# Kernel optimization log

Measured on AMD Instinct MI355X. Metric: run time of the kernel, lower is better.

Reference implementation:

```python
import jax, jax.numpy as jnp
import numpy as np

B, L, C, N, TN = 1, 256, 128, 4, 4
CH = N * C  # 512, flattened hidden for routing projections
EPS = 1.1920929e-07  # torch.finfo(float32).eps (RMSNorm default eps)
LN_EPS = 1e-5
N_SINKHORN = 20  # training-mode iteration count


def sinkhorn_knopp(raw, n_iters):
    # raw: [..., n, n] real-valued logits -> doubly-stochastic matrix
    M = jnp.exp(raw)
    for _ in range(n_iters):
        M = M / jnp.sum(M, axis=-1, keepdims=True)  # row normalize
        M = M / jnp.sum(M, axis=-2, keepdims=True)  # col normalize
    return M


def setup_inputs() -> dict:
    key = jax.random.key(0)
    ks = jax.random.split(key, 8)
    s = 0.02
    eye = jnp.eye(N, dtype=jnp.float32)
    b_res = 2.0 * eye + (-2.0) * (1.0 - eye)
    return {
        "p": jax.random.normal(ks[0], (B, L, L, C), jnp.float32),
        "p_mask": jnp.ones((B, L, L), jnp.float32),
        "W_pre": jax.random.normal(ks[1], (N, CH), jnp.float32) * s,
        "W_post": jax.random.normal(ks[2], (N, CH), jnp.float32) * s,
        "W_res": jax.random.normal(ks[3], (N * N, CH), jnp.float32) * s,
        "b_pre": jnp.zeros((1, N), jnp.float32),
        "b_post": jnp.zeros((1, N), jnp.float32),
        "b_res": b_res,
        "alpha_pre": jnp.asarray(0.01, jnp.float32),
        "alpha_post": jnp.asarray(0.01, jnp.float32),
        "alpha_res": jnp.asarray(0.01, jnp.float32),
        "ln_g": jnp.ones((C,), jnp.float32),
        "ln_b": jnp.zeros((C,), jnp.float32),
        "W1": jax.random.normal(ks[4], (TN * C, C), jnp.float32) * s,
        "b1": jnp.zeros((TN * C,), jnp.float32),
        "W2": jax.random.normal(ks[5], (C, TN * C), jnp.float32) * s,
        "b2": jnp.zeros((C,), jnp.float32),
    }


def reference(p, p_mask, W_pre, W_post, W_res, b_pre, b_post, b_res,
              alpha_pre, alpha_post, alpha_res, ln_g, ln_b, W1, b1, W2, b2):
    # expand_input: [B,L,L,C] -> [B,L,L,n,C]
    x = jnp.broadcast_to(p[..., None, :], (B, L, L, N, C))
    # --- compute_mappings ---
    xf = x.reshape(B, L, L, CH)
    xn = xf * jax.lax.rsqrt(jnp.mean(xf * xf, axis=-1, keepdims=True) + EPS)
    H_pre_dyn = jnp.tanh(xn @ W_pre.T)                      # [B,L,L,n]
    H_post_dyn = jnp.tanh(xn @ W_post.T)                    # [B,L,L,n]
    H_res_dyn = jnp.tanh(xn @ W_res.T).reshape(B, L, L, N, N)
    H_pre = jax.nn.sigmoid(alpha_pre * H_pre_dyn + b_pre)   # [B,L,L,n]
    H_post = 2.0 * jax.nn.sigmoid(alpha_post * H_post_dyn + b_post)
    H_res = sinkhorn_knopp(alpha_res * H_res_dyn + b_res, N_SINKHORN)  # [B,L,L,n,n]
    # contract: H_pre [B,L,L,1,n] @ x [B,L,L,n,C] -> [B,L,L,C]
    p_c = jnp.einsum('blkn,blknc->blkc', H_pre, x)
    # --- PairTransition (LN -> Linear -> ReLU -> Linear, masked) ---
    mu = jnp.mean(p_c, axis=-1, keepdims=True)
    var = jnp.mean(jnp.square(p_c - mu), axis=-1, keepdims=True)
    m = (p_c - mu) * jax.lax.rsqrt(var + LN_EPS) * ln_g + ln_b
    h = jax.nn.relu(m @ W1.T + b1)                          # [B,L,L,TN*C]
    p_t = (h @ W2.T + b2) * p_mask[..., None]
    p_updated = p_c + p_t
    # expand back: H_post^T [B,L,L,n,1] * p_updated [B,L,L,1,C]
    p_expanded = H_post[..., :, None] * p_updated[..., None, :]
    # residual mixing: [B,L,L,n,n] @ [B,L,L,n,C]
    p_residual = jnp.einsum('blkmn,blknc->blkmc', H_res, x)
    return p_residual + p_expanded  # [B,L,L,n,C]
```

## Files before the change

### kernel.cpp

```cpp
#include <hip/hip_runtime.h>
#include <stdint.h>

#define LLTOT 65536
#define CDIM  128
#define TPIX  32

typedef float f32x4  __attribute__((ext_vector_type(4)));
typedef float f32x16 __attribute__((ext_vector_type(16)));
typedef short s16x8  __attribute__((ext_vector_type(8)));

#define MFMA16(a, b, c) __builtin_amdgcn_mfma_f32_16x16x32_bf16((a), (b), (c), 0, 0, 0)
#define MFMA32(a, b, c) __builtin_amdgcn_mfma_f32_32x32x16_bf16((a), (b), (c), 0, 0, 0)

#define RPAD 132

__device__ __align__(16) unsigned short g_wefff[2 * 4 * 64 * 8];
__device__ __align__(16) unsigned short g_w1gf[32 * 4 * 64 * 8];
__device__ __align__(16) unsigned short g_w2f [4 * 32 * 64 * 8];
__device__ __align__(16) float  g_hA[512];
__device__ __align__(16) float  g_w1gs[512];

__device__ __forceinline__ unsigned short f2bf(float f) {
    union { float f; uint32_t u; } v; v.f = f;
    uint32_t u = v.u;
    return (unsigned short)((u + 0x7FFFu + ((u >> 16) & 1u)) >> 16);
}
__device__ __forceinline__ uint32_t pack2(float a, float b) {
    uint32_t r;
    asm("v_cvt_pk_bf16_f32 %0, %1, %2" : "=v"(r) : "v"(a), "v"(b));
    return r;
}
__device__ __forceinline__ float bf2f(uint32_t lo16) { return __uint_as_float(lo16 << 16); }

__device__ __forceinline__ float fast_tanh(float x) {
    float cx = fminf(fmaxf(x, -10.f), 10.f);
    float e = __expf(2.f * cx);
    return (e - 1.f) * __builtin_amdgcn_rcpf(e + 1.f);
}
__device__ __forceinline__ float fast_sig(float z) {
    return __builtin_amdgcn_rcpf(1.f + __expf(-z));
}

__global__ void prep_kernel(const float* __restrict__ Wpre, const float* __restrict__ Wpost,
                            const float* __restrict__ Wres, const float* __restrict__ W1,
                            const float* __restrict__ W2, const float* __restrict__ ln_g,
                            const float* __restrict__ ln_b, const float* __restrict__ b1) {
    int b = blockIdx.x, t = threadIdx.x;
    if (b == 264) {
        int j = t;
        float sg = 0.f, sb = 0.f;
        const float* row = W1 + j * 128;
        #pragma unroll 4
        for (int c = 0; c < 128; c += 4) {
            float4 wv = *(const float4*)(row + c);
            float4 gv = *(const float4*)(ln_g + c);
            float4 bv = *(const float4*)(ln_b + c);
            sg += wv.x*gv.x + wv.y*gv.y + wv.z*gv.z + wv.w*gv.w;
            sb += wv.x*bv.x + wv.y*bv.y + wv.z*bv.z + wv.w*bv.w;
        }
        g_hA[j]   = b1[j] + sb;
        g_w1gs[j] = sg;
        return;
    }
    int idx = b * 512 + t;
    if (idx < 4096) {
        int e = idx & 7, lane = (idx >> 3) & 63, kk = (idx >> 9) & 3, tile = idx >> 11;
        int o = tile * 16 + (lane & 15);
        int c = kk * 32 + (lane >> 4) * 8 + e;
        float v = 0.f;
        if (o < 4)        v = Wpre[o*512+c] + Wpre[o*512+128+c] + Wpre[o*512+256+c] + Wpre[o*512+384+c];
        else if (o < 8)   { int j = o - 4;  v = Wpost[j*512+c] + Wpost[j*512+128+c] + Wpost[j*512+256+c] + Wpost[j*512+384+c]; }
        else if (o < 24)  { int j = o - 8;  v = Wres[j*512+c] + Wres[j*512+128+c] + Wres[j*512+256+c] + Wres[j*512+384+c]; }
        g_wefff[idx] = f2bf(v);
    } else if (idx < 69632) {
        int d = idx - 4096;
        int e = d & 7, lane = (d >> 3) & 63, kk = (d >> 9) & 3, jt = d >> 11;
        int j = jt * 16 + (lane & 15);
        int c = kk * 32 + (lane >> 4) * 8 + e;
        g_w1gf[d] = f2bf(W1[j * 128 + c] * ln_g[c]);
    } else if (idx < 135168) {
        int d = idx - 69632;
        int e = d & 7, lane = (d >> 3) & 63, kk = (d >> 9) & 31, ct = (d >> 14) & 3;
        int c = ct * 32 + (lane & 31);
        int k = kk * 16 + (lane >> 5) * 8 + e;
        g_w2f[d] = f2bf(W2[c * 512 + k]);
    }
}

__global__ void __launch_bounds__(512, 2) fused_kernel(
    const float* __restrict__ p, const float* __restrict__ p_mask,
    const float* __restrict__ b_pre, const float* __restrict__ b_post, const float* __restrict__ b_res,
    const float* __restrict__ a_pre, const float* __restrict__ a_post, const float* __restrict__ a_res,
    const float* __restrict__ b2g, float* __restrict__ out)
{
    __shared__ __align__(16) unsigned short pf_lds[8 * 64 * 8];
    __shared__ __align__(16) unsigned short h32[32 * 64 * 8];
    __shared__ __align__(16) float redA[32 * RPAD];
    __shared__ __align__(16) float redB[32 * RPAD];
    __shared__ __align__(16) float A_s[128], B_s[128];
    __shared__ __align__(16) float2 simi_s[32];
    __shared__ __align__(16) float rms_s[32], mu_s[32], var_s[32];

    const int t = threadIdx.x;
    const int w = t >> 6, l = t & 63, lr = l & 15, lk = l >> 4;
    const size_t base = (size_t)blockIdx.x * TPIX;

    s16x8 aw01[8];
    #pragma unroll
    for (int kk = 0; kk < 2; ++kk)
        #pragma unroll
        for (int jt = 0; jt < 4; ++jt)
            aw01[kk * 4 + jt] = *(const s16x8*)(g_w1gf + ((size_t)((w * 4 + jt) * 4 + kk) * 64 + l) * 8);

    {
        int pix32 = t >> 4, ci = t & 15;
        const float* src = p + (base + pix32) * 128 + ci * 8;
        float4 va = *(const float4*)src;
        float4 vb = *(const float4*)(src + 4);
        float s  = va.x + va.y + va.z + va.w + vb.x + vb.y + vb.z + vb.w;
        float ss = va.x*va.x + va.y*va.y + va.z*va.z + va.w*va.w
                 + vb.x*vb.x + vb.y*vb.y + vb.z*vb.z + vb.w*vb.w;
        s += __shfl_xor(s, 1); ss += __shfl_xor(ss, 1);
        s += __shfl_xor(s, 2); ss += __shfl_xor(ss, 2);
        s += __shfl_xor(s, 4); ss += __shfl_xor(ss, 4);
        s += __shfl_xor(s, 8); ss += __shfl_xor(ss, 8);
        if (ci == 0) {
            float mu = s * (1.f / 128.f), mq = ss * (1.f / 128.f);
            rms_s[pix32] = rsqrtf(mq + 1.1920929e-07f);
            mu_s[pix32]  = mu;
            var_s[pix32] = mq - mu * mu;
        }
        uint4 u;
        u.x = pack2(va.x, va.y);
        u.y = pack2(va.z, va.w);
        u.z = pack2(vb.x, vb.y);
        u.w = pack2(vb.z, vb.w);
        uint32_t a16 = (uint32_t)((((pix32 >> 4) * 4 + (ci >> 2)) * 512
                     + ((pix32 & 15) + 16 * (ci & 3)) * 8));
        *(uint4*)(pf_lds + a16) = u;
    }
    __syncthreads();

    float M0 = 0.f, M1 = 0.f, M2 = 0.f, M3 = 0.f, sp = 0.f, hpm = 0.f;
    int mrow = 0, pix = 0;

    if (w < 2) {
        const int g = lk, pixl = lr;
        const size_t gpix = base + w * 16 + pixl;
        float apre = a_pre[0], apost = a_post[0], ares = a_res[0];
        float msk = p_mask[gpix];
        float bp0 = b_pre[0], bp1 = b_pre[1], bp2 = b_pre[2], bp3 = b_pre[3];
        float bq0 = b_post[0], bq1 = b_post[1], bq2 = b_post[2], bq3 = b_post[3];
        mrow = (g + 2) & 3;
        float br0 = b_res[mrow*4+0], br1 = b_res[mrow*4+1], br2 = b_res[mrow*4+2], br3 = b_res[mrow*4+3];

        float rv = rms_s[w * 16 + pixl];

        f32x4 y1 = {0.f, 0.f, 0.f, 0.f}, y2 = {0.f, 0.f, 0.f, 0.f};
        #pragma unroll
        for (int kk = 0; kk < 4; ++kk) {
            s16x8 bfr = *(const s16x8*)(pf_lds + (size_t)(w * 4 + kk) * 512 + l * 8);
            s16x8 a0 = *(const s16x8*)(g_wefff + ((size_t)(kk) * 64 + l) * 8);
            s16x8 a1 = *(const s16x8*)(g_wefff + ((size_t)(4 + kk) * 64 + l) * 8);
            y1 = MFMA16(a0, bfr, y1);
            y2 = MFMA16(a1, bfr, y2);
        }
        #pragma unroll
        for (int r = 0; r < 4; ++r) { y1[r] *= rv; y2[r] *= rv; }

        float sp_loc = fast_sig(apre * fast_tanh(y1[0]) + bp0)
                     + fast_sig(apre * fast_tanh(y1[1]) + bp1)
                     + fast_sig(apre * fast_tanh(y1[2]) + bp2)
                     + fast_sig(apre * fast_tanh(y1[3]) + bp3);
        sp = __shfl(sp_loc, pixl);

        float hp0 = 2.f * fast_sig(apost * fast_tanh(y1[0]) + bq0);
        float hp1 = 2.f * fast_sig(apost * fast_tanh(y1[1]) + bq1);
        float hp2 = 2.f * fast_sig(apost * fast_tanh(y1[2]) + bq2);
        float hp3 = 2.f * fast_sig(apost * fast_tanh(y1[3]) + bq3);

        bool lo = g < 2;
        M0 = __expf(ares * fast_tanh(lo ? y2[0] : y1[0]) + br0);
        M1 = __expf(ares * fast_tanh(lo ? y2[1] : y1[1]) + br1);
        M2 = __expf(ares * fast_tanh(lo ? y2[2] : y1[2]) + br2);
        M3 = __expf(ares * fast_tanh(lo ? y2[3] : y1[3]) + br3);

        float h0b = __shfl(hp0, pixl + 16);
        float h1b = __shfl(hp1, pixl + 16);
        float h2b = __shfl(hp2, pixl + 16);
        float h3b = __shfl(hp3, pixl + 16);
        hpm = (mrow & 2) ? ((mrow & 1) ? h3b : h2b) : ((mrow & 1) ? h1b : h0b);

        pix = w * 16 + pixl;
        B_s[pix * 4 + mrow] = hpm * msk;
        if (l < 16) {
            int px = w * 16 + lr;
            float istd = rsqrtf(sp * sp * var_s[px] + 1e-5f);
            simi_s[px] = make_float2(sp * istd, sp * mu_s[px] * istd);
        }
    }
    __syncthreads();

    if (w < 2) {
        #pragma unroll 1
        for (int it = 0; it < 20; ++it) {
            float ri = __builtin_amdgcn_rcpf(M0 + M1 + M2 + M3);
            M0 *= ri; M1 *= ri; M2 *= ri; M3 *= ri;
            float c0 = M0, c1 = M1, c2 = M2, c3 = M3;
            c0 += __shfl_xor(c0, 16); c1 += __shfl_xor(c1, 16); c2 += __shfl_xor(c2, 16); c3 += __shfl_xor(c3, 16);
            c0 += __shfl_xor(c0, 32); c1 += __shfl_xor(c1, 32); c2 += __shfl_xor(c2, 32); c3 += __shfl_xor(c3, 32);
            M0 *= __builtin_amdgcn_rcpf(c0); M1 *= __builtin_amdgcn_rcpf(c1);
            M2 *= __builtin_amdgcn_rcpf(c2); M3 *= __builtin_amdgcn_rcpf(c3);
        }
        float rm = M0 + M1 + M2 + M3;
        A_s[pix * 4 + mrow] = rm + hpm * sp;
    }

    s16x8 pfr[2][4];
    #pragma unroll
    for (int it = 0; it < 2; ++it)
        #pragma unroll
        for (int kk = 0; kk < 4; ++kk)
            pfr[it][kk] = *(const s16x8*)(pf_lds + (size_t)(it * 4 + kk) * 512 + l * 8);

    f32x4 acc1[4][2] = {};
    #pragma unroll
    for (int kk = 0; kk < 2; ++kk)
        #pragma unroll
        for (int jt = 0; jt < 4; ++jt) {
            s16x8 a = aw01[kk * 4 + jt];
            acc1[jt][0] = MFMA16(a, pfr[0][kk], acc1[jt][0]);
            acc1[jt][1] = MFMA16(a, pfr[1][kk], acc1[jt][1]);
        }
    #pragma unroll
    for (int kk = 2; kk < 4; ++kk)
        #pragma unroll
        for (int jt = 0; jt < 4; ++jt) {
            s16x8 a = *(const s16x8*)(g_w1gf + ((size_t)((w * 4 + jt) * 4 + kk) * 64 + l) * 8);
            acc1[jt][0] = MFMA16(a, pfr[0][kk], acc1[jt][0]);
            acc1[jt][1] = MFMA16(a, pfr[1][kk], acc1[jt][1]);
        }

    {
        float2 sim0 = simi_s[lr];
        float2 sim1 = simi_s[16 + lr];
        #pragma unroll
        for (int jt = 0; jt < 4; ++jt) {
            int j0 = w * 64 + jt * 16 + lk * 4;
            float4 wg = *(const float4*)(g_w1gs + j0);
            float4 ha = *(const float4*)(g_hA + j0);
            #pragma unroll
            for (int it = 0; it < 2; ++it) {
                float si = it ? sim1.x : sim0.x;
                float mi = it ? sim1.y : sim0.y;
                f32x4 v = acc1[jt][it];
                float h0 = fmaxf(fmaf(si, v[0], fmaf(-mi, wg.x, ha.x)), 0.f);
                float h1 = fmaxf(fmaf(si, v[1], fmaf(-mi, wg.y, ha.y)), 0.f);
                float h2 = fmaxf(fmaf(si, v[2], fmaf(-mi, wg.z, ha.z)), 0.f);
                float h3 = fmaxf(fmaf(si, v[3], fmaf(-mi, wg.w, ha.w)), 0.f);
                uint2 uu;
                uu.x = pack2(h0, h1);
                uu.y = pack2(h2, h3);
                uint32_t addr = (uint32_t)((w * 4 + jt) * 1024
                              + (it * 16 + lr + 32 * (lk >> 1)) * 16 + (lk & 1) * 8);
                *(uint2*)((char*)h32 + addr) = uu;
            }
        }
    }
    __syncthreads();

    {
        const int ct = w & 3, kh = w >> 2;
        f32x16 acc2 = {0.f,0.f,0.f,0.f, 0.f,0.f,0.f,0.f, 0.f,0.f,0.f,0.f, 0.f,0.f,0.f,0.f};
        #pragma unroll 4
        for (int kk2 = 0; kk2 < 16; ++kk2) {
            int ks = kh * 16 + kk2;
            s16x8 a = *(const s16x8*)(g_w2f + ((size_t)(ct * 32 + ks) * 64 + l) * 8);
            s16x8 b = *(const s16x8*)(h32 + (size_t)ks * 512 + l * 8);
            acc2 = MFMA32(a, b, acc2);
        }
        float* red = kh ? redB : redA;
        int pixd = l & 31;
        #pragma unroll
        for (int q = 0; q < 4; ++q) {
            f32x4 v = {acc2[4*q+0], acc2[4*q+1], acc2[4*q+2], acc2[4*q+3]};
            int c = ct * 32 + 8 * q + 4 * (l >> 5);
            *(f32x4*)(red + pixd * RPAD + c) = v;
        }
    }
    __syncthreads();

    const int c0 = w * 16 + lk * 4;
    float4 b2v = *(const float4*)(b2g + c0);
    #pragma unroll
    for (int it = 0; it < 2; ++it) {
        int i = it * 16 + lr;
        f32x4 Av = *(const f32x4*)(A_s + i * 4);
        f32x4 Bv = *(const f32x4*)(B_s + i * 4);
        f32x4 Da = *(const f32x4*)(redA + i * RPAD + c0);
        f32x4 Db = *(const f32x4*)(redB + i * RPAD + c0);
        const unsigned short* pe = pf_lds
            + ((size_t)(it * 4 + (w >> 1)) * 64 + ((w & 1) * 2 + (lk >> 1)) * 16 + lr) * 8
            + (lk & 1) * 4;
        uint2 pb = *(const uint2*)pe;
        float p0 = bf2f(pb.x & 0xffffu), p1 = __uint_as_float(pb.x & 0xffff0000u);
        float p2 = bf2f(pb.y & 0xffffu), p3 = __uint_as_float(pb.y & 0xffff0000u);
        float d0 = Da[0] + Db[0] + b2v.x;
        float d1 = Da[1] + Db[1] + b2v.y;
        float d2 = Da[2] + Db[2] + b2v.z;
        float d3 = Da[3] + Db[3] + b2v.w;
        float* og = out + (base + i) * 512 + c0;
        #pragma unroll
        for (int m = 0; m < 4; ++m) {
            f32x4 o;
            o[0] = Av[m] * p0 + Bv[m] * d0;
            o[1] = Av[m] * p1 + Bv[m] * d1;
            o[2] = Av[m] * p2 + Bv[m] * d2;
            o[3] = Av[m] * p3 + Bv[m] * d3;
            *(f32x4*)(og + m * 128) = o;
        }
    }
}

extern "C" void kernel_launch(void* const* d_in, const int* in_sizes, int n_in,
                              void* d_out, int out_size, void* d_ws, size_t ws_size,
                              hipStream_t stream) {
    const float* p      = (const float*)d_in[0];
    const float* p_mask = (const float*)d_in[1];
    const float* W_pre  = (const float*)d_in[2];
    const float* W_post = (const float*)d_in[3];
    const float* W_res  = (const float*)d_in[4];
    const float* b_pre  = (const float*)d_in[5];
    const float* b_post = (const float*)d_in[6];
    const float* b_res  = (const float*)d_in[7];
    const float* a_pre  = (const float*)d_in[8];
    const float* a_post = (const float*)d_in[9];
    const float* a_res  = (const float*)d_in[10];
    const float* ln_g   = (const float*)d_in[11];
    const float* ln_b   = (const float*)d_in[12];
    const float* W1     = (const float*)d_in[13];
    const float* b1     = (const float*)d_in[14];
    const float* W2     = (const float*)d_in[15];
    const float* b2     = (const float*)d_in[16];
    float* out = (float*)d_out;

    prep_kernel<<<265, 512, 0, stream>>>(W_pre, W_post, W_res, W1, W2, ln_g, ln_b, b1);
    fused_kernel<<<2048, 512, 0, stream>>>(p, p_mask, b_pre, b_post, b_res,
                                           a_pre, a_post, a_res, b2, out);
}
```

Measured before the change: 71.07 us.

## Compute second GEMM with 16x16 MFMA full-K per wave, drop LDS reduction

Changes the second linear layer (W2) from 32x32 MFMA tiles with a split-K over two wave halves to 16x16x32 MFMA tiles. In the new layout each wave owns 16 output channels across the full K of 512, so results land directly in registers in the same layout the epilogue needs. This removes the redA/redB LDS reduction buffers, their stores and loads, and one __syncthreads. In exchange, each wave runs a longer serial MFMA chain over K and the W2 weights and hidden-activation LDS buffer are re-laid out to match.

```diff
diff --git a/kernel.cpp b/kernel.cpp
--- a/kernel.cpp
+++ b/kernel.cpp
@@ -6,17 +6,13 @@
 #define TPIX  32
 
 typedef float f32x4  __attribute__((ext_vector_type(4)));
-typedef float f32x16 __attribute__((ext_vector_type(16)));
 typedef short s16x8  __attribute__((ext_vector_type(8)));
 
 #define MFMA16(a, b, c) __builtin_amdgcn_mfma_f32_16x16x32_bf16((a), (b), (c), 0, 0, 0)
-#define MFMA32(a, b, c) __builtin_amdgcn_mfma_f32_32x32x16_bf16((a), (b), (c), 0, 0, 0)
-
-#define RPAD 132
 
 __device__ __align__(16) unsigned short g_wefff[2 * 4 * 64 * 8];
 __device__ __align__(16) unsigned short g_w1gf[32 * 4 * 64 * 8];
-__device__ __align__(16) unsigned short g_w2f [4 * 32 * 64 * 8];
+__device__ __align__(16) unsigned short g_w2f16[16 * 8 * 64 * 8];
 __device__ __align__(16) float  g_hA[512];
 __device__ __align__(16) float  g_w1gs[512];
 
@@ -80,10 +76,10 @@
         g_w1gf[d] = f2bf(W1[j * 128 + c] * ln_g[c]);
     } else if (idx < 135168) {
         int d = idx - 69632;
-        int e = d & 7, lane = (d >> 3) & 63, kk = (d >> 9) & 31, ct = (d >> 14) & 3;
-        int c = ct * 32 + (lane & 31);
-        int k = kk * 16 + (lane >> 5) * 8 + e;
-        g_w2f[d] = f2bf(W2[c * 512 + k]);
+        int e = d & 7, lane = (d >> 3) & 63, ct = (d >> 9) & 7, ksg = d >> 12;
+        int c = ct * 16 + (lane & 15);
+        int k = ksg * 32 + (lane >> 4) * 8 + e;
+        g_w2f16[d] = f2bf(W2[c * 512 + k]);
     }
 }
 
@@ -93,10 +89,8 @@
     const float* __restrict__ a_pre, const float* __restrict__ a_post, const float* __restrict__ a_res,
     const float* __restrict__ b2g, float* __restrict__ out)
 {
-    __shared__ __align__(16) unsigned short pf_lds[8 * 64 * 8];
-    __shared__ __align__(16) unsigned short h32[32 * 64 * 8];
-    __shared__ __align__(16) float redA[32 * RPAD];
-    __shared__ __align__(16) float redB[32 * RPAD];
+    __shared__ __align__(16) unsigned short pf_lds[8 * 512];
+    __shared__ __align__(16) unsigned short h16[32 * 512];
     __shared__ __align__(16) float A_s[128], B_s[128];
     __shared__ __align__(16) float2 simi_s[32];
     __shared__ __align__(16) float rms_s[32], mu_s[32], var_s[32];
@@ -249,6 +243,8 @@
             int j0 = w * 64 + jt * 16 + lk * 4;
             float4 wg = *(const float4*)(g_w1gs + j0);
             float4 ha = *(const float4*)(g_hA + j0);
+            int ksg = w * 2 + (jt >> 1);
+            int laneB = lr + 16 * ((jt & 1) * 2 + (lk >> 1));
             #pragma unroll
             for (int it = 0; it < 2; ++it) {
                 float si = it ? sim1.x : sim0.x;
@@ -261,34 +257,21 @@
                 uint2 uu;
                 uu.x = pack2(h0, h1);
                 uu.y = pack2(h2, h3);
-                uint32_t addr = (uint32_t)((w * 4 + jt) * 1024
-                              + (it * 16 + lr + 32 * (lk >> 1)) * 16 + (lk & 1) * 8);
-                *(uint2*)((char*)h32 + addr) = uu;
+                *(uint2*)(h16 + (size_t)(ksg * 2 + it) * 512 + laneB * 8 + (lk & 1) * 4) = uu;
             }
         }
     }
     __syncthreads();
 
-    {
-        const int ct = w & 3, kh = w >> 2;
-        f32x16 acc2 = {0.f,0.f,0.f,0.f, 0.f,0.f,0.f,0.f, 0.f,0.f,0.f,0.f, 0.f,0.f,0.f,0.f};
-        #pragma unroll 4
-        for (int kk2 = 0; kk2 < 16; ++kk2) {
-            int ks = kh * 16 + kk2;
-            s16x8 a = *(const s16x8*)(g_w2f + ((size_t)(ct * 32 + ks) * 64 + l) * 8);
-            s16x8 b = *(const s16x8*)(h32 + (size_t)ks * 512 + l * 8);
-            acc2 = MFMA32(a, b, acc2);
-        }
-        float* red = kh ? redB : redA;
-        int pixd = l & 31;
-        #pragma unroll
-        for (int q = 0; q < 4; ++q) {
-            f32x4 v = {acc2[4*q+0], acc2[4*q+1], acc2[4*q+2], acc2[4*q+3]};
-            int c = ct * 32 + 8 * q + 4 * (l >> 5);
-            *(f32x4*)(red + pixd * RPAD + c) = v;
-        }
-    }
-    __syncthreads();
+    f32x4 acc2[2] = {};
+    #pragma unroll 4
+    for (int ksg = 0; ksg < 16; ++ksg) {
+        s16x8 a  = *(const s16x8*)(g_w2f16 + ((size_t)(ksg * 8 + w) * 64 + l) * 8);
+        s16x8 b0 = *(const s16x8*)(h16 + (size_t)(ksg * 2 + 0) * 512 + l * 8);
+        s16x8 b1 = *(const s16x8*)(h16 + (size_t)(ksg * 2 + 1) * 512 + l * 8);
+        acc2[0] = MFMA16(a, b0, acc2[0]);
+        acc2[1] = MFMA16(a, b1, acc2[1]);
+    }
 
     const int c0 = w * 16 + lk * 4;
     float4 b2v = *(const float4*)(b2g + c0);
@@ -297,18 +280,14 @@
         int i = it * 16 + lr;
         f32x4 Av = *(const f32x4*)(A_s + i * 4);
         f32x4 Bv = *(const f32x4*)(B_s + i * 4);
-        f32x4 Da = *(const f32x4*)(redA + i * RPAD + c0);
-        f32x4 Db = *(const f32x4*)(redB + i * RPAD + c0);
         const unsigned short* pe = pf_lds
             + ((size_t)(it * 4 + (w >> 1)) * 64 + ((w & 1) * 2 + (lk >> 1)) * 16 + lr) * 8
             + (lk & 1) * 4;
         uint2 pb = *(const uint2*)pe;
         float p0 = bf2f(pb.x & 0xffffu), p1 = __uint_as_float(pb.x & 0xffff0000u);
         float p2 = bf2f(pb.y & 0xffffu), p3 = __uint_as_float(pb.y & 0xffff0000u);
-        float d0 = Da[0] + Db[0] + b2v.x;
-        float d1 = Da[1] + Db[1] + b2v.y;
-        float d2 = Da[2] + Db[2] + b2v.z;
-        float d3 = Da[3] + Db[3] + b2v.w;
+        float d0 = acc2[it][0] + b2v.x, d1 = acc2[it][1] + b2v.y;
+        float d2 = acc2[it][2] + b2v.z, d3 = acc2[it][3] + b2v.w;
         float* og = out + (base + i) * 512 + c0;
         #pragma unroll
         for (int m = 0; m < 4; ++m) {
```

After: 70.17 us, median of 2. No clear change (-1.3%).
